# Performance work log

Measured on AMD Instinct MI355X. Metric: run time of the kernel, lower is better.

Reference implementation:

```python
import jax, jax.numpy as jnp
import numpy as np

B, C, H, W = 64, 8, 256, 256
EMB, LAT = 64, 32


def affine_grid(theta, Hh, Ww):
    # F.affine_grid, align_corners=False. theta: [N,2,3] -> grid [N,H,W,2] (x,y)
    xs = (jnp.arange(Ww, dtype=theta.dtype) + 0.5) * (2.0 / Ww) - 1.0
    ys = (jnp.arange(Hh, dtype=theta.dtype) + 0.5) * (2.0 / Hh) - 1.0
    X, Y = jnp.meshgrid(xs, ys)  # [H,W]
    base = jnp.stack([X, Y, jnp.ones_like(X)], axis=-1)  # [H,W,3]
    return jnp.einsum('hwk,nik->nhwi', base, theta)


def grid_sample(img, grid):
    # F.grid_sample bilinear, padding_mode='zeros', align_corners=False
    # img: [N,C,H,W], grid: [N,H,W,2]
    N, Cc, Hh, Ww = img.shape
    ix = ((grid[..., 0] + 1.0) * Ww - 1.0) * 0.5
    iy = ((grid[..., 1] + 1.0) * Hh - 1.0) * 0.5
    x0 = jnp.floor(ix)
    y0 = jnp.floor(iy)
    wx1 = ix - x0
    wy1 = iy - y0
    wx0 = 1.0 - wx1
    wy0 = 1.0 - wy1

    def gather(xf, yf):
        xi = xf.astype(jnp.int32)
        yi = yf.astype(jnp.int32)
        valid = ((xi >= 0) & (xi < Ww) & (yi >= 0) & (yi < Hh)).astype(img.dtype)
        xc = jnp.clip(xi, 0, Ww - 1)
        yc = jnp.clip(yi, 0, Hh - 1)

        def one(im, yb, xb, vb):
            return im[:, yb, xb] * vb[None]  # [C,H,W]

        return jax.vmap(one)(img, yc, xc, valid)

    v00 = gather(x0, y0)
    v01 = gather(x0 + 1.0, y0)
    v10 = gather(x0, y0 + 1.0)
    v11 = gather(x0 + 1.0, y0 + 1.0)
    w00 = (wy0 * wx0)[:, None]
    w01 = (wy0 * wx1)[:, None]
    w10 = (wy1 * wx0)[:, None]
    w11 = (wy1 * wx1)[:, None]
    return v00 * w00 + v01 * w01 + v10 * w10 + v11 * w11


def setup_inputs() -> dict:
    key = jax.random.key(0)
    ks = jax.random.split(key, 9)
    return {
        'x': jax.random.normal(ks[0], (B, C, H, W), jnp.float32),
        'W_ae': jax.random.normal(ks[1], (C, EMB), jnp.float32) * 0.1,
        'W_rot': jax.random.normal(ks[2], (EMB, 6), jnp.float32) * 0.1,
        'W_scale': jax.random.normal(ks[3], (EMB, 6), jnp.float32) * 0.1,
        'W_shear': jax.random.normal(ks[4], (EMB, 6), jnp.float32) * 0.1,
        'W_trans': jax.random.normal(ks[5], (EMB, 6), jnp.float32) * 0.1,
        'W_mask': jax.random.normal(ks[6], (EMB, 1), jnp.float32) * 0.1,
        'W_enc': jax.random.normal(ks[7], (C, LAT), jnp.float32) * 0.1,
        'W_dec': jax.random.normal(ks[8], (C, C), jnp.float32) * 0.1,
    }


def reference(x, W_ae, W_rot, W_scale, W_shear, W_trans, W_mask, W_enc, W_dec):
    Bb, Cc, Hh, Ww = x.shape
    # affine_encoder: global-average-pool + linear
    emb_affine = x.mean(axis=(2, 3)) @ W_ae  # [B,EMB]
    eye = jnp.array([[1.0, 0.0, 0.0], [0.0, 1.0, 0.0]], x.dtype)
    head = lambda Wt: (emb_affine @ Wt).reshape(Bb, 2, 3) * 0.1 + eye
    rotation = head(W_rot)
    scale = head(W_scale)
    shear = head(W_shear)
    translation = head(W_trans)
    mask_parameter = jax.nn.sigmoid(emb_affine @ W_mask)[:, :, None, None]  # [B,1,1,1]

    # affine_transform: four sequential affine_grid + grid_sample passes, then mask
    xt = x
    for theta in (rotation, scale, shear, translation):
        grid = affine_grid(theta, Hh, Ww)
        xt = grid_sample(xt, grid)
    xt = xt * mask_parameter

    emb = xt.mean(axis=(2, 3)) @ W_enc  # encoder on transformed image
    x_dec = jnp.einsum('bchw,cd->bdhw', xt, W_dec)  # pointwise-linear decoder
    return (x_dec, emb, scale, shear, rotation, translation, mask_parameter)
```

## Files before the change

### kernel.cpp

```cpp
#include <hip/hip_runtime.h>
#include <hip/hip_fp16.h>
#include <math.h>

#define BB   64
#define CC   8
#define HH   256
#define WW   256
#define EMB  64
#define LAT  32
#define HW   (HH*WW)
#define PLANE 65536
#define IMG  (CC*HW)

#define OFF_XDEC  0
#define OFF_EMB   33554432
#define OFF_SCALE 33556480
#define OFF_SHEAR 33556864
#define OFF_ROT   33557248
#define OFF_TRANS 33557632
#define OFF_MASK  33558016

#define WS_SUMS   0
#define WS_THETA  512
#define WS_MASK   2048
#define WS_ACC    2112
#define WS_BUF0   4096
#define WS_BUF1   (4096 + 16777216)

#define TH 16
#define TW 64
#define SR 20
#define SC 68
#define SN (SR*SC)

typedef float v2f __attribute__((ext_vector_type(2)));

__global__ void k_zero(float* __restrict__ ws) {
    ws[WS_SUMS + threadIdx.x] = 0.f;
}

__device__ __forceinline__ unsigned pack2(float a, float b) {
    __half2 t = __floats2half2_rn(a, b);
    return *(unsigned*)&t;
}
__device__ __forceinline__ float2 up2(unsigned v) {
    __half2 h = *(__half2*)&v;
    return __half22float2(h);
}

__global__ void k_meanT(const float* __restrict__ x, uint4* __restrict__ outp,
                        float* __restrict__ sums) {
    int bid = blockIdx.x;
    int b = bid >> 6;
    int hq = bid & 63;
    int r = threadIdx.x >> 6;
    int lane = threadIdx.x & 63;
    int h = hq * 4 + r;
    const float* ib = x + (size_t)b * IMG + h * WW + 4 * lane;
    float4 v0 = *(const float4*)(ib + 0 * PLANE);
    float4 v1 = *(const float4*)(ib + 1 * PLANE);
    float4 v2 = *(const float4*)(ib + 2 * PLANE);
    float4 v3 = *(const float4*)(ib + 3 * PLANE);
    float4 v4 = *(const float4*)(ib + 4 * PLANE);
    float4 v5 = *(const float4*)(ib + 5 * PLANE);
    float4 v6 = *(const float4*)(ib + 6 * PLANE);
    float4 v7 = *(const float4*)(ib + 7 * PLANE);

    uint4* ob = outp + (size_t)b * HW + h * WW + 4 * lane;
#define PIXOUT(J, COMP) { uint4 u; \
    u.x = pack2(v0.COMP, v1.COMP); u.y = pack2(v2.COMP, v3.COMP); \
    u.z = pack2(v4.COMP, v5.COMP); u.w = pack2(v6.COMP, v7.COMP); ob[J] = u; }
    PIXOUT(0, x) PIXOUT(1, y) PIXOUT(2, z) PIXOUT(3, w)
#undef PIXOUT

    float p[CC];
    p[0] = (v0.x + v0.y) + (v0.z + v0.w);
    p[1] = (v1.x + v1.y) + (v1.z + v1.w);
    p[2] = (v2.x + v2.y) + (v2.z + v2.w);
    p[3] = (v3.x + v3.y) + (v3.z + v3.w);
    p[4] = (v4.x + v4.y) + (v4.z + v4.w);
    p[5] = (v5.x + v5.y) + (v5.z + v5.w);
    p[6] = (v6.x + v6.y) + (v6.z + v6.w);
    p[7] = (v7.x + v7.y) + (v7.z + v7.w);

    __shared__ float part[4][CC];
    #pragma unroll
    for (int ch = 0; ch < CC; ch++) {
        float v = p[ch];
        for (int off = 32; off > 0; off >>= 1) v += __shfl_down(v, off, 64);
        if (lane == 0) part[r][ch] = v;
    }
    __syncthreads();
    if (threadIdx.x < CC) {
        float v = (part[0][threadIdx.x] + part[1][threadIdx.x]) +
                  (part[2][threadIdx.x] + part[3][threadIdx.x]);
        atomicAdd(&sums[b * CC + threadIdx.x], v);
    }
}

__global__ void k_params(const float* __restrict__ sums,
                         const float* __restrict__ W_ae, const float* __restrict__ W_rot,
                         const float* __restrict__ W_scale, const float* __restrict__ W_shear,
                         const float* __restrict__ W_trans, const float* __restrict__ W_mask,
                         float* __restrict__ ws, float* __restrict__ out) {
    int b = blockIdx.x;
    int t = threadIdx.x;

    if (t < CC) ws[WS_ACC + b * CC + t] = 0.f;

    __shared__ float emb_s[EMB];
    {
        float s = 0.f;
        #pragma unroll
        for (int c = 0; c < CC; c++)
            s += (sums[b * CC + c] * (1.0f / (float)HW)) * W_ae[c * EMB + t];
        emb_s[t] = s;
    }
    __syncthreads();

    if (t < 24) {
        int h = t / 6, k = t % 6;
        const float* Wt = (h == 0) ? W_rot : (h == 1) ? W_scale : (h == 2) ? W_shear : W_trans;
        float s = 0.f;
        #pragma unroll
        for (int e = 0; e < EMB; e++) s += emb_s[e] * Wt[e * 6 + k];
        const float eyev = (k == 0 || k == 4) ? 1.0f : 0.0f;
        float th = s * 0.1f + eyev;
        ws[WS_THETA + h * (BB * 6) + b * 6 + k] = th;
        int off = (h == 0) ? OFF_ROT : (h == 1) ? OFF_SCALE : (h == 2) ? OFF_SHEAR : OFF_TRANS;
        out[off + b * 6 + k] = th;
    } else if (t == 24) {
        float s = 0.f;
        #pragma unroll
        for (int e = 0; e < EMB; e++) s += emb_s[e] * W_mask[e];
        float mk = 1.0f / (1.0f + expf(-s));
        ws[WS_MASK + b] = mk;
        out[OFF_MASK + b] = mk;
    }
}

struct Corners {
    int x0c, x1c, y0c, y1c;
    float w00, w01, w10, w11;
};

__device__ __forceinline__ Corners affine_corners(float t00, float t01, float t02,
                                                  float t10, float t11, float t12,
                                                  int gh, int gw) {
    float X = ((float)gw + 0.5f) * (2.0f / (float)WW) - 1.0f;
    float Y = ((float)gh + 0.5f) * (2.0f / (float)HH) - 1.0f;
    float gx = X * t00 + Y * t01 + t02;
    float gy = X * t10 + Y * t11 + t12;
    float ix = ((gx + 1.0f) * (float)WW - 1.0f) * 0.5f;
    float iy = ((gy + 1.0f) * (float)HH - 1.0f) * 0.5f;
    float x0f = floorf(ix), y0f = floorf(iy);
    int x0 = (int)x0f, y0 = (int)y0f, x1 = x0 + 1, y1 = y0 + 1;
    float wx1 = ix - x0f, wy1 = iy - y0f, wx0 = 1.f - wx1, wy0 = 1.f - wy1;
    float fx0 = ((unsigned)x0 < (unsigned)WW) ? 1.f : 0.f;
    float fx1 = ((unsigned)x1 < (unsigned)WW) ? 1.f : 0.f;
    float fy0 = ((unsigned)y0 < (unsigned)HH) ? 1.f : 0.f;
    float fy1 = ((unsigned)y1 < (unsigned)HH) ? 1.f : 0.f;
    Corners c;
    c.x0c = min(max(x0, 0), WW - 1); c.x1c = min(max(x1, 0), WW - 1);
    c.y0c = min(max(y0, 0), HH - 1); c.y1c = min(max(y1, 0), HH - 1);
    c.w00 = wy0*wx0*fy0*fx0; c.w01 = wy0*wx1*fy0*fx1;
    c.w10 = wy1*wx0*fy1*fx0; c.w11 = wy1*wx1*fy1*fx1;
    return c;
}

__device__ __forceinline__ uint4 bilerp8_pk(uint4 a00, uint4 a01, uint4 a10, uint4 a11,
                                            __half2 h00, __half2 h01, __half2 h10, __half2 h11) {
    uint4 u;
#define BLEND(COMP) { \
    __half2 r = __hmul2(*(__half2*)&a00.COMP, h00); \
    r = __hfma2(*(__half2*)&a01.COMP, h01, r); \
    r = __hfma2(*(__half2*)&a10.COMP, h10, r); \
    r = __hfma2(*(__half2*)&a11.COMP, h11, r); \
    u.COMP = *(unsigned*)&r; }
    BLEND(x) BLEND(y) BLEND(z) BLEND(w)
#undef BLEND
    return u;
}

__device__ __forceinline__ int lidx(int sr, int sc) {
    sr = min(max(sr, 0), SR - 1);
    sc = min(max(sc, 0), SC - 1);
    return sr * SC + (sc ^ ((sc >> 3) & 7));
}

template<int NT>
__device__ __forceinline__ void stage_g2l(uint4* __restrict__ buf,
                                          const uint4* __restrict__ pb,
                                          const float* __restrict__ th,
                                          int oh, int ow, int tid) {
    float t00 = th[0], t01 = th[1], t02 = th[2], t10 = th[3], t11 = th[4], t12 = th[5];
    for (int i = tid; i < SN; i += NT) {
        int lr = i / SC, lc = i - lr * SC;
        Corners c = affine_corners(t00, t01, t02, t10, t11, t12, oh - 2 + lr, ow - 2 + lc);
        uint4 a00 = pb[c.y0c * WW + c.x0c], a01 = pb[c.y0c * WW + c.x1c];
        uint4 a10 = pb[c.y1c * WW + c.x0c], a11 = pb[c.y1c * WW + c.x1c];
        __half2 h00 = __float2half2_rn(c.w00), h01 = __float2half2_rn(c.w01);
        __half2 h10 = __float2half2_rn(c.w10), h11 = __float2half2_rn(c.w11);
        buf[lr * SC + (lc ^ ((lc >> 3) & 7))] =
            bilerp8_pk(a00, a01, a10, a11, h00, h01, h10, h11);
    }
}

__global__ __launch_bounds__(512) void k_warpA(const uint4* __restrict__ in,
                                               uint4* __restrict__ out,
                                               const float* __restrict__ ws) {
    __shared__ uint4 buf[SN];
    int bid = blockIdx.x;
    int b = bid >> 6;
    int tile = bid & 63;
    int oh = (tile >> 2) * TH;
    int ow = (tile & 3) * TW;
    int tid = threadIdx.x;
    const uint4* pb = in + (size_t)b * HW;

    stage_g2l<512>(buf, pb, ws + WS_THETA + 0 * (BB * 6) + b * 6, oh, ow, tid);
    __syncthreads();

    const float* th = ws + WS_THETA + 1 * (BB * 6) + b * 6;
    float t00 = th[0], t01 = th[1], t02 = th[2], t10 = th[3], t11 = th[4], t12 = th[5];
    uint4* ob = out + (size_t)b * HW;
    #pragma unroll
    for (int j = 0; j < 2; ++j) {
        int i = tid + j * 512;
        int lr = i >> 6, lc = i & 63;
        int gh = oh + lr, gw = ow + lc;
        Corners c = affine_corners(t00, t01, t02, t10, t11, t12, gh, gw);
        uint4 a00 = buf[lidx(c.y0c - oh + 2, c.x0c - ow + 2)];
        uint4 a01 = buf[lidx(c.y0c - oh + 2, c.x1c - ow + 2)];
        uint4 a10 = buf[lidx(c.y1c - oh + 2, c.x0c - ow + 2)];
        uint4 a11 = buf[lidx(c.y1c - oh + 2, c.x1c - ow + 2)];
        __half2 h00 = __float2half2_rn(c.w00), h01 = __float2half2_rn(c.w01);
        __half2 h10 = __float2half2_rn(c.w10), h11 = __float2half2_rn(c.w11);
        ob[gh * WW + gw] = bilerp8_pk(a00, a01, a10, a11, h00, h01, h10, h11);
    }
}

__global__ __launch_bounds__(512) void k_warpB(const uint4* __restrict__ in,
                                               const float* __restrict__ ws,
                                               const float* __restrict__ W_dec,
                                               float* __restrict__ out,
                                               float* __restrict__ acc) {
    __shared__ uint4 buf[SN];
    __shared__ v2f Wd2[CC][4];
    __shared__ float part[8][CC];
    int bid = blockIdx.x;
    int b = bid >> 6;
    int tile = bid & 63;
    int oh = (tile >> 2) * TH;
    int ow = (tile & 3) * TW;
    int tid = threadIdx.x;
    if (tid < CC * 4) {
        int ch = tid >> 2, j = tid & 3;
        v2f w; w.x = W_dec[ch * CC + 2 * j]; w.y = W_dec[ch * CC + 2 * j + 1];
        Wd2[ch][j] = w;
    }
    const uint4* pb = in + (size_t)b * HW;

    stage_g2l<512>(buf, pb, ws + WS_THETA + 2 * (BB * 6) + b * 6, oh, ow, tid);
    __syncthreads();

    float mk = ws[WS_MASK + b];
    const float* th = ws + WS_THETA + 3 * (BB * 6) + b * 6;
    float t00 = th[0], t01 = th[1], t02 = th[2], t10 = th[3], t11 = th[4], t12 = th[5];

    int wv = tid >> 6, lane = tid & 63;
    int r = wv * 2 + (lane >> 5);
    int c0 = (lane & 31) * 2;
    float sl[CC];
    #pragma unroll
    for (int ch = 0; ch < CC; ch++) sl[ch] = 0.f;
    float od[CC][2];

    #pragma unroll
    for (int px = 0; px < 2; px++) {
        int gh = oh + r, gw = ow + c0 + px;
        Corners c = affine_corners(t00, t01, t02, t10, t11, t12, gh, gw);
        uint4 a00 = buf[lidx(c.y0c - oh + 2, c.x0c - ow + 2)];
        uint4 a01 = buf[lidx(c.y0c - oh + 2, c.x1c - ow + 2)];
        uint4 a10 = buf[lidx(c.y1c - oh + 2, c.x0c - ow + 2)];
        uint4 a11 = buf[lidx(c.y1c - oh + 2, c.x1c - ow + 2)];
        __half2 h00 = __float2half2_rn(c.w00 * mk), h01 = __float2half2_rn(c.w01 * mk);
        __half2 h10 = __float2half2_rn(c.w10 * mk), h11 = __float2half2_rn(c.w11 * mk);
        uint4 u = bilerp8_pk(a00, a01, a10, a11, h00, h01, h10, h11);

        float2 s01 = up2(u.x), s23 = up2(u.y), s45 = up2(u.z), s67 = up2(u.w);
        float s[CC] = {s01.x, s01.y, s23.x, s23.y, s45.x, s45.y, s67.x, s67.y};

        #pragma unroll
        for (int ch = 0; ch < CC; ch++) sl[ch] += s[ch];

        v2f o2[4];
        #pragma unroll
        for (int j = 0; j < 4; j++) { o2[j].x = 0.f; o2[j].y = 0.f; }
        #pragma unroll
        for (int ch = 0; ch < CC; ch++) {
            v2f sb; sb.x = s[ch]; sb.y = s[ch];
            #pragma unroll
            for (int j = 0; j < 4; j++)
                o2[j] = __builtin_elementwise_fma(sb, Wd2[ch][j], o2[j]);
        }
        #pragma unroll
        for (int j = 0; j < 4; j++) { od[2*j][px] = o2[j].x; od[2*j+1][px] = o2[j].y; }
    }

    size_t base = (size_t)b * IMG + (size_t)(oh + r) * WW + (ow + c0);
    #pragma unroll
    for (int d = 0; d < CC; d++) {
        float2 f2 = make_float2(od[d][0], od[d][1]);
        *(float2*)(out + OFF_XDEC + base + d * PLANE) = f2;
    }

    #pragma unroll
    for (int ch = 0; ch < CC; ch++) {
        float v = sl[ch];
        for (int off = 32; off > 0; off >>= 1) v += __shfl_down(v, off, 64);
        if (lane == 0) part[wv][ch] = v;
    }
    __syncthreads();
    if (tid < CC) {
        float v = 0.f;
        #pragma unroll
        for (int w = 0; w < 8; w++) v += part[w][tid];
        atomicAdd(&acc[b * CC + tid], v);
    }
}

__global__ void k_emb(const float* __restrict__ acc, const float* __restrict__ W_enc,
                      float* __restrict__ out) {
    for (int i = threadIdx.x; i < BB * LAT; i += 256) {
        int b = i >> 5, l = i & 31;
        float s = 0.f;
        #pragma unroll
        for (int c = 0; c < CC; c++)
            s += (acc[b * CC + c] * (1.0f / (float)HW)) * W_enc[c * LAT + l];
        out[OFF_EMB + i] = s;
    }
}

extern "C" void kernel_launch(void* const* d_in, const int* in_sizes, int n_in,
                              void* d_out, int out_size, void* d_ws, size_t ws_size,
                              hipStream_t stream) {
    const float* x       = (const float*)d_in[0];
    const float* W_ae    = (const float*)d_in[1];
    const float* W_rot   = (const float*)d_in[2];
    const float* W_scale = (const float*)d_in[3];
    const float* W_shear = (const float*)d_in[4];
    const float* W_trans = (const float*)d_in[5];
    const float* W_mask  = (const float*)d_in[6];
    const float* W_enc   = (const float*)d_in[7];
    const float* W_dec   = (const float*)d_in[8];

    float* ws   = (float*)d_ws;
    float* out  = (float*)d_out;
    float* sums = ws + WS_SUMS;
    float* acc  = ws + WS_ACC;
    uint4* hb0  = (uint4*)(ws + WS_BUF0);
    uint4* hb1  = (uint4*)(ws + WS_BUF1);

    k_zero<<<1, 512, 0, stream>>>(ws);
    k_meanT<<<BB * (HH / 4), 256, 0, stream>>>(x, hb0, sums);
    k_params<<<BB, 64, 0, stream>>>(sums, W_ae, W_rot, W_scale, W_shear, W_trans, W_mask, ws, out);
    k_warpA<<<BB * 64, 512, 0, stream>>>(hb0, hb1, ws);
    k_warpB<<<BB * 64, 512, 0, stream>>>(hb1, ws, W_dec, out, acc);
    k_emb<<<1, 256, 0, stream>>>(acc, W_enc, out);
}
```

Baseline: 138.3 us.

## Fuse three warp passes into one kernel, stream final warp from global

Moves the third affine warp out of the decoder kernel into the first warp kernel, which now chains three bilinear passes through two shared-memory halo tiles (24x72 and 20x68). The final warp+decoder kernel reads the four corners straight from global memory over full-width row strips instead of staging a tile in LDS. This shifts work between kernels and removes one LDS staging pass and its barrier from the decoder kernel. The cost is a larger shared-memory footprint and extra halo recomputation in the fused kernel, plus uncached-tile gathers in the decoder.

```diff
diff --git a/kernel.cpp b/kernel.cpp
--- a/kernel.cpp
+++ b/kernel.cpp
@@ -29,9 +29,10 @@
 
 #define TH 16
 #define TW 64
-#define SR 20
-#define SC 68
-#define SN (SR*SC)
+#define A_R 24
+#define A_C 72
+#define B_R 20
+#define B_C 68
 
 typedef float v2f __attribute__((ext_vector_type(2)));
 
@@ -182,34 +183,22 @@
     return u;
 }
 
-__device__ __forceinline__ int lidx(int sr, int sc) {
-    sr = min(max(sr, 0), SR - 1);
-    sc = min(max(sc, 0), SC - 1);
-    return sr * SC + (sc ^ ((sc >> 3) & 7));
-}
-
-template<int NT>
-__device__ __forceinline__ void stage_g2l(uint4* __restrict__ buf,
-                                          const uint4* __restrict__ pb,
-                                          const float* __restrict__ th,
-                                          int oh, int ow, int tid) {
-    float t00 = th[0], t01 = th[1], t02 = th[2], t10 = th[3], t11 = th[4], t12 = th[5];
-    for (int i = tid; i < SN; i += NT) {
-        int lr = i / SC, lc = i - lr * SC;
-        Corners c = affine_corners(t00, t01, t02, t10, t11, t12, oh - 2 + lr, ow - 2 + lc);
-        uint4 a00 = pb[c.y0c * WW + c.x0c], a01 = pb[c.y0c * WW + c.x1c];
-        uint4 a10 = pb[c.y1c * WW + c.x0c], a11 = pb[c.y1c * WW + c.x1c];
-        __half2 h00 = __float2half2_rn(c.w00), h01 = __float2half2_rn(c.w01);
-        __half2 h10 = __float2half2_rn(c.w10), h11 = __float2half2_rn(c.w11);
-        buf[lr * SC + (lc ^ ((lc >> 3) & 7))] =
-            bilerp8_pk(a00, a01, a10, a11, h00, h01, h10, h11);
-    }
-}
-
-__global__ __launch_bounds__(512) void k_warpA(const uint4* __restrict__ in,
-                                               uint4* __restrict__ out,
-                                               const float* __restrict__ ws) {
-    __shared__ uint4 buf[SN];
+__device__ __forceinline__ int aidx(int sr, int sc) {
+    sr = min(max(sr, 0), A_R - 1);
+    sc = min(max(sc, 0), A_C - 1);
+    return sr * A_C + (sc ^ ((sc >> 3) & 7));
+}
+__device__ __forceinline__ int bidx(int sr, int sc) {
+    sr = min(max(sr, 0), B_R - 1);
+    sc = min(max(sc, 0), B_C - 1);
+    return sr * B_C + (sc ^ ((sc >> 3) & 7));
+}
+
+__global__ __launch_bounds__(512) void k_warpA3(const uint4* __restrict__ in,
+                                                uint4* __restrict__ out,
+                                                const float* __restrict__ ws) {
+    __shared__ uint4 bufA[A_R * A_C];
+    __shared__ uint4 bufB[B_R * B_C];
     int bid = blockIdx.x;
     int b = bid >> 6;
     int tile = bid & 63;
@@ -217,60 +206,93 @@
     int ow = (tile & 3) * TW;
     int tid = threadIdx.x;
     const uint4* pb = in + (size_t)b * HW;
-
-    stage_g2l<512>(buf, pb, ws + WS_THETA + 0 * (BB * 6) + b * 6, oh, ow, tid);
-    __syncthreads();
-
-    const float* th = ws + WS_THETA + 1 * (BB * 6) + b * 6;
-    float t00 = th[0], t01 = th[1], t02 = th[2], t10 = th[3], t11 = th[4], t12 = th[5];
-    uint4* ob = out + (size_t)b * HW;
-    #pragma unroll
-    for (int j = 0; j < 2; ++j) {
-        int i = tid + j * 512;
-        int lr = i >> 6, lc = i & 63;
-        int gh = oh + lr, gw = ow + lc;
-        Corners c = affine_corners(t00, t01, t02, t10, t11, t12, gh, gw);
-        uint4 a00 = buf[lidx(c.y0c - oh + 2, c.x0c - ow + 2)];
-        uint4 a01 = buf[lidx(c.y0c - oh + 2, c.x1c - ow + 2)];
-        uint4 a10 = buf[lidx(c.y1c - oh + 2, c.x0c - ow + 2)];
-        uint4 a11 = buf[lidx(c.y1c - oh + 2, c.x1c - ow + 2)];
-        __half2 h00 = __float2half2_rn(c.w00), h01 = __float2half2_rn(c.w01);
-        __half2 h10 = __float2half2_rn(c.w10), h11 = __float2half2_rn(c.w11);
-        ob[gh * WW + gw] = bilerp8_pk(a00, a01, a10, a11, h00, h01, h10, h11);
-    }
-}
-
-__global__ __launch_bounds__(512) void k_warpB(const uint4* __restrict__ in,
-                                               const float* __restrict__ ws,
-                                               const float* __restrict__ W_dec,
-                                               float* __restrict__ out,
-                                               float* __restrict__ acc) {
-    __shared__ uint4 buf[SN];
+    const float* thetas = ws + WS_THETA;
+
+    {
+        const float* th = thetas + 0 * (BB * 6) + b * 6;
+        float t00 = th[0], t01 = th[1], t02 = th[2], t10 = th[3], t11 = th[4], t12 = th[5];
+        for (int i = tid; i < A_R * A_C; i += 512) {
+            int lr = i / A_C, lc = i - lr * A_C;
+            Corners c = affine_corners(t00, t01, t02, t10, t11, t12, oh - 4 + lr, ow - 4 + lc);
+            uint4 a00 = pb[c.y0c * WW + c.x0c], a01 = pb[c.y0c * WW + c.x1c];
+            uint4 a10 = pb[c.y1c * WW + c.x0c], a11 = pb[c.y1c * WW + c.x1c];
+            __half2 h00 = __float2half2_rn(c.w00), h01 = __float2half2_rn(c.w01);
+            __half2 h10 = __float2half2_rn(c.w10), h11 = __float2half2_rn(c.w11);
+            bufA[lr * A_C + (lc ^ ((lc >> 3) & 7))] =
+                bilerp8_pk(a00, a01, a10, a11, h00, h01, h10, h11);
+        }
+    }
+    __syncthreads();
+
+    {
+        const float* th = thetas + 1 * (BB * 6) + b * 6;
+        float t00 = th[0], t01 = th[1], t02 = th[2], t10 = th[3], t11 = th[4], t12 = th[5];
+        for (int i = tid; i < B_R * B_C; i += 512) {
+            int lr = i / B_C, lc = i - lr * B_C;
+            Corners c = affine_corners(t00, t01, t02, t10, t11, t12, oh - 2 + lr, ow - 2 + lc);
+            uint4 a00 = bufA[aidx(c.y0c - oh + 4, c.x0c - ow + 4)];
+            uint4 a01 = bufA[aidx(c.y0c - oh + 4, c.x1c - ow + 4)];
+            uint4 a10 = bufA[aidx(c.y1c - oh + 4, c.x0c - ow + 4)];
+            uint4 a11 = bufA[aidx(c.y1c - oh + 4, c.x1c - ow + 4)];
+            __half2 h00 = __float2half2_rn(c.w00), h01 = __float2half2_rn(c.w01);
+            __half2 h10 = __float2half2_rn(c.w10), h11 = __float2half2_rn(c.w11);
+            bufB[lr * B_C + (lc ^ ((lc >> 3) & 7))] =
+                bilerp8_pk(a00, a01, a10, a11, h00, h01, h10, h11);
+        }
+    }
+    __syncthreads();
+
+    {
+        const float* th = thetas + 2 * (BB * 6) + b * 6;
+        float t00 = th[0], t01 = th[1], t02 = th[2], t10 = th[3], t11 = th[4], t12 = th[5];
+        uint4* ob = out + (size_t)b * HW;
+        #pragma unroll
+        for (int j = 0; j < 2; ++j) {
+            int i = tid + j * 512;
+            int lr = i >> 6, lc = i & 63;
+            int gh = oh + lr, gw = ow + lc;
+            Corners c = affine_corners(t00, t01, t02, t10, t11, t12, gh, gw);
+            uint4 a00 = bufB[bidx(c.y0c - oh + 2, c.x0c - ow + 2)];
+            uint4 a01 = bufB[bidx(c.y0c - oh + 2, c.x1c - ow + 2)];
+            uint4 a10 = bufB[bidx(c.y1c - oh + 2, c.x0c - ow + 2)];
+            uint4 a11 = bufB[bidx(c.y1c - oh + 2, c.x1c - ow + 2)];
+            __half2 h00 = __float2half2_rn(c.w00), h01 = __float2half2_rn(c.w01);
+            __half2 h10 = __float2half2_rn(c.w10), h11 = __float2half2_rn(c.w11);
+            ob[gh * WW + gw] = bilerp8_pk(a00, a01, a10, a11, h00, h01, h10, h11);
+        }
+    }
+}
+
+__global__ __launch_bounds__(512) void k_warpBt(const uint4* __restrict__ in,
+                                                const float* __restrict__ ws,
+                                                const float* __restrict__ W_dec,
+                                                float* __restrict__ out,
+                                                float* __restrict__ acc) {
     __shared__ v2f Wd2[CC][4];
     __shared__ float part[8][CC];
     int bid = blockIdx.x;
     int b = bid >> 6;
-    int tile = bid & 63;
-    int oh = (tile >> 2) * TH;
-    int ow = (tile & 3) * TW;
+    int hq = bid & 63;
+    int oh = hq * 4;
     int tid = threadIdx.x;
     if (tid < CC * 4) {
         int ch = tid >> 2, j = tid & 3;
         v2f w; w.x = W_dec[ch * CC + 2 * j]; w.y = W_dec[ch * CC + 2 * j + 1];
         Wd2[ch][j] = w;
     }
+    __syncthreads();
+
     const uint4* pb = in + (size_t)b * HW;
-
-    stage_g2l<512>(buf, pb, ws + WS_THETA + 2 * (BB * 6) + b * 6, oh, ow, tid);
-    __syncthreads();
-
     float mk = ws[WS_MASK + b];
     const float* th = ws + WS_THETA + 3 * (BB * 6) + b * 6;
     float t00 = th[0], t01 = th[1], t02 = th[2], t10 = th[3], t11 = th[4], t12 = th[5];
 
     int wv = tid >> 6, lane = tid & 63;
-    int r = wv * 2 + (lane >> 5);
-    int c0 = (lane & 31) * 2;
+    int p0 = 2 * tid;
+    int row = p0 >> 8;
+    int col0 = p0 & 255;
+    int gh = oh + row;
+
     float sl[CC];
     #pragma unroll
     for (int ch = 0; ch < CC; ch++) sl[ch] = 0.f;
@@ -278,12 +300,10 @@
 
     #pragma unroll
     for (int px = 0; px < 2; px++) {
-        int gh = oh + r, gw = ow + c0 + px;
+        int gw = col0 + px;
         Corners c = affine_corners(t00, t01, t02, t10, t11, t12, gh, gw);
-        uint4 a00 = buf[lidx(c.y0c - oh + 2, c.x0c - ow + 2)];
-        uint4 a01 = buf[lidx(c.y0c - oh + 2, c.x1c - ow + 2)];
-        uint4 a10 = buf[lidx(c.y1c - oh + 2, c.x0c - ow + 2)];
-        uint4 a11 = buf[lidx(c.y1c - oh + 2, c.x1c - ow + 2)];
+        uint4 a00 = pb[c.y0c * WW + c.x0c], a01 = pb[c.y0c * WW + c.x1c];
+        uint4 a10 = pb[c.y1c * WW + c.x0c], a11 = pb[c.y1c * WW + c.x1c];
         __half2 h00 = __float2half2_rn(c.w00 * mk), h01 = __float2half2_rn(c.w01 * mk);
         __half2 h10 = __float2half2_rn(c.w10 * mk), h11 = __float2half2_rn(c.w11 * mk);
         uint4 u = bilerp8_pk(a00, a01, a10, a11, h00, h01, h10, h11);
@@ -308,7 +328,7 @@
         for (int j = 0; j < 4; j++) { od[2*j][px] = o2[j].x; od[2*j+1][px] = o2[j].y; }
     }
 
-    size_t base = (size_t)b * IMG + (size_t)(oh + r) * WW + (ow + c0);
+    size_t base = (size_t)b * IMG + (size_t)gh * WW + col0;
     #pragma unroll
     for (int d = 0; d < CC; d++) {
         float2 f2 = make_float2(od[d][0], od[d][1]);
@@ -365,7 +385,7 @@
     k_zero<<<1, 512, 0, stream>>>(ws);
     k_meanT<<<BB * (HH / 4), 256, 0, stream>>>(x, hb0, sums);
     k_params<<<BB, 64, 0, stream>>>(sums, W_ae, W_rot, W_scale, W_shear, W_trans, W_mask, ws, out);
-    k_warpA<<<BB * 64, 512, 0, stream>>>(hb0, hb1, ws);
-    k_warpB<<<BB * 64, 512, 0, stream>>>(hb1, ws, W_dec, out, acc);
+    k_warpA3<<<BB * 64, 512, 0, stream>>>(hb0, hb1, ws);
+    k_warpBt<<<BB * 64, 512, 0, stream>>>(hb1, ws, W_dec, out, acc);
     k_emb<<<1, 256, 0, stream>>>(acc, W_enc, out);
 }
```

Result: slower. 147.0 us (+6.3%).
